# Performance work log

Measured on AMD Instinct MI355X. Metric: run time of the kernel, lower is better.

The kernel has to match this reference:

```python
import jax, jax.numpy as jnp
import numpy as np

BN_EPS = 1e-5

def _conv3x3(x, w):
    # x: [N,C,H,W], w: [O,I,3,3], stride 1, padding 1, no bias
    return jax.lax.conv_general_dilated(
        x, w, window_strides=(1, 1), padding=((1, 1), (1, 1)),
        dimension_numbers=("NCHW", "OIHW", "NCHW"))

def _batchnorm(x, gamma, beta):
    # training-mode BN: batch statistics over (N,H,W)
    mean = jnp.mean(x, axis=(0, 2, 3), keepdims=True)
    var = jnp.mean(jnp.square(x - mean), axis=(0, 2, 3), keepdims=True)
    inv = jax.lax.rsqrt(var + BN_EPS)
    g = gamma.reshape(1, -1, 1, 1)
    b = beta.reshape(1, -1, 1, 1)
    return (x - mean) * inv * g + b

def setup_inputs() -> dict:
    key = jax.random.key(0)
    ks = jax.random.split(key, 3)
    x = jax.random.normal(ks[0], (32, 64, 128, 128), dtype=jnp.float32)
    # He-style scaled 3x3 conv kernels
    w1 = jax.random.normal(ks[1], (64, 64, 3, 3), dtype=jnp.float32) * (2.0 / (64 * 9)) ** 0.5
    w2 = jax.random.normal(ks[2], (64, 64, 3, 3), dtype=jnp.float32) * (2.0 / (64 * 9)) ** 0.5
    return {
        "x": x, "w1": w1, "w2": w2,
        "bn1_gamma": jnp.ones((64,), jnp.float32),
        "bn1_beta": jnp.zeros((64,), jnp.float32),
        "bn2_gamma": jnp.ones((64,), jnp.float32),
        "bn2_beta": jnp.zeros((64,), jnp.float32),
    }

def reference(x, w1, w2, bn1_gamma, bn1_beta, bn2_gamma, bn2_beta):
    out = _batchnorm(_conv3x3(x, w1), bn1_gamma, bn1_beta)
    out = _conv3x3(out, w2)
    out = out + x  # option 'A', stride=1, planes[2]==planes[0] -> identity shortcut
    return _batchnorm(out, bn2_gamma, bn2_beta)
```

## Files before the change

kernel.cpp:

```cpp
#include <hip/hip_runtime.h>
#include <hip/hip_bf16.h>

#define NB 32
#define CH 64
#define HH 128
#define WW 128
#define HW (HH*WW)
#define CHW (CH*HW)
#define NCHW (NB*CHW)
#define CNT_PER_CH ((float)(NB*HW))

typedef __attribute__((ext_vector_type(8)))  short short8;
typedef __attribute__((ext_vector_type(16))) float f32x16;

__device__ __forceinline__ unsigned short f2bf(float f) {
  unsigned u = __builtin_bit_cast(unsigned, f);
  u += 0x7fffu + ((u >> 16) & 1u);
  return (unsigned short)(u >> 16);
}

__device__ __forceinline__ void gld_lds16(const void* g, void* s) {
  __builtin_amdgcn_global_load_lds(
      (const __attribute__((address_space(1))) unsigned int*)g,
      (__attribute__((address_space(3))) unsigned int*)s, 16, 0, 0);
}

__global__ __launch_bounds__(256) void t1_pack(const float* __restrict__ x,
                                               unsigned short* __restrict__ xb) {
  __shared__ __align__(16) unsigned short tmp[CH * WW];
  const int bid = blockIdx.x;
  const int tid = threadIdx.x;
  const float* src = x + (size_t)(bid >> 7) * CHW + (size_t)(bid & 127) * WW;
  for (int i = tid; i < 2048; i += 256) {
    const int ci = i >> 5, wq = i & 31;
    const float4 v = *(const float4*)(src + (size_t)ci * HW + wq * 4);
    unsigned short* d = &tmp[ci * WW + wq * 4];
    d[0] = f2bf(v.x); d[1] = f2bf(v.y); d[2] = f2bf(v.z); d[3] = f2bf(v.w);
  }
  __syncthreads();
  unsigned short* dst = xb + (size_t)bid * 8192;
  for (int i = tid; i < 1024; i += 256) {
    const int cb = i >> 7, w = i & 127;
    const unsigned short* s = &tmp[cb * 8 * WW + w];
    uint4 o;
    o.x = (unsigned)s[0]      | ((unsigned)s[WW]     << 16);
    o.y = (unsigned)s[2*WW]   | ((unsigned)s[3*WW]   << 16);
    o.z = (unsigned)s[4*WW]   | ((unsigned)s[5*WW]   << 16);
    o.w = (unsigned)s[6*WW]   | ((unsigned)s[7*WW]   << 16);
    *(uint4*)(dst + ((size_t)cb * WW + w) * 8) = o;
  }
}

__global__ __launch_bounds__(256) void pack_w(const float* __restrict__ w,
                                              const float* __restrict__ s1,
                                              const float* __restrict__ b1,
                                              unsigned short* __restrict__ wpk,
                                              float* __restrict__ tabs) {
  const int tid = threadIdx.x;
  for (int idx = tid; idx < 36864; idx += 256) {
    const int f = idx >> 9, l = (idx >> 3) & 63, r = idx & 7;
    const int m = f & 1, kq = (f >> 1) & 3, t = f >> 3;
    const int co = (l & 31) + 32 * m;
    const int ci = kq * 16 + (l >> 5) * 8 + r;
    float v = w[co * 576 + ci * 9 + t];
    if (s1) v *= s1[ci];
    wpk[idx] = f2bf(v);
  }
  if (tabs != nullptr && tid < 64) {
    const int co = tid;
    float tb[9];
    for (int t = 0; t < 9; ++t) {
      float a = 0.f;
      for (int ci = 0; ci < 64; ++ci) a += w[co * 576 + ci * 9 + t] * b1[ci];
      tb[t] = a;
    }
    tabs[0*64+co] = tb[0]+tb[1]+tb[2]+tb[3]+tb[4]+tb[5]+tb[6]+tb[7]+tb[8];
    tabs[1*64+co] = tb[0]+tb[1]+tb[2];
    tabs[2*64+co] = tb[6]+tb[7]+tb[8];
    tabs[3*64+co] = tb[0]+tb[3]+tb[6];
    tabs[4*64+co] = tb[2]+tb[5]+tb[8];
    tabs[5*64+co] = tb[0]; tabs[6*64+co] = tb[2];
    tabs[7*64+co] = tb[6]; tabs[8*64+co] = tb[8];
  }
}

template <bool IS2>
__global__ __launch_bounds__(256, 2)
void conv_mfma(const unsigned short* __restrict__ inb,
               const unsigned short* __restrict__ wpack,
               const float* __restrict__ tabs,
               const float* __restrict__ resid,
               unsigned short* __restrict__ outb,
               float* __restrict__ outf,
               float* __restrict__ psum, float* __restrict__ psq) {
  __shared__ __align__(16) unsigned short A[3][8][130][8];
  const int tid = threadIdx.x, bid = blockIdx.x;
  const int n = bid >> 7, h = bid & 127;
  const int wv = tid >> 6, lane = tid & 63;
  const int half = lane >> 5, lp = lane & 31;
  const int m  = wv & 1;
  const int nb = (wv >> 1) << 1;

  for (int q = wv; q < 48; q += 4) {
    const int rr = q >> 4, cb = (q >> 1) & 7, w0 = (q & 1) << 6;
    const int hr = h - 1 + rr;
    if ((unsigned)hr < 128u) {
      const unsigned short* g =
          inb + ((((size_t)n * 128 + hr) * 8 + cb) << 10) + (size_t)(w0 + lane) * 8;
      gld_lds16(g, &A[rr][cb][1 + w0][0]);
    } else {
      *(uint4*)&A[rr][cb][1 + w0 + lane][0] = make_uint4(0, 0, 0, 0);
    }
  }
  if (tid < 48) {
    const int rr = tid >> 4, cb = (tid >> 1) & 7, s = (tid & 1) ? 129 : 0;
    *(uint4*)&A[rr][cb][s][0] = make_uint4(0, 0, 0, 0);
  }

  short8 wr[36];
#pragma unroll
  for (int i = 0; i < 36; ++i) {
    const int f = ((i >> 2) << 3) + ((i & 3) << 1) + m;
    wr[i] = *(const short8*)(wpack + (size_t)f * 512 + (size_t)lane * 8);
  }
  __syncthreads();

  f32x16 acc0 = {}; f32x16 acc1 = {};
#pragma unroll
  for (int kh = 0; kh < 3; ++kh) {
#pragma unroll
    for (int kw = 0; kw < 3; ++kw) {
#pragma unroll
      for (int kq = 0; kq < 4; ++kq) {
        const short8 wf = wr[(kh * 3 + kw) * 4 + kq];
        const int cb = kq * 2 + half;
        const short8 b0 = *(const short8*)&A[kh][cb][nb * 32 + lp + kw][0];
        const short8 b1 = *(const short8*)&A[kh][cb][(nb + 1) * 32 + lp + kw][0];
        acc0 = __builtin_amdgcn_mfma_f32_32x32x16_bf16(wf, b0, acc0, 0, 0, 0);
        acc1 = __builtin_amdgcn_mfma_f32_32x32x16_bf16(wf, b1, acc1, 0, 0, 0);
      }
    }
  }

  if (!IS2) {
    unsigned short* dst = outb + ((size_t)bid << 13);
#pragma unroll
    for (int nt = 0; nt < 2; ++nt) {
      const f32x16& a = nt ? acc1 : acc0;
      const int px = (nb + nt) * 32 + lp;
#pragma unroll
      for (int rq = 0; rq < 4; ++rq) {
        uint2 pk;
        pk.x = (unsigned)f2bf(a[rq*4+0]) | ((unsigned)f2bf(a[rq*4+1]) << 16);
        pk.y = (unsigned)f2bf(a[rq*4+2]) | ((unsigned)f2bf(a[rq*4+3]) << 16);
        *(uint2*)(dst + (((size_t)(rq + 4*m)) << 10) + (size_t)px * 8 + half * 4) = pk;
      }
    }
  } else {
    const bool bh0 = (h == 0), bh1 = (h == 127);
#pragma unroll
    for (int nt = 0; nt < 2; ++nt) {
      f32x16& a = nt ? acc1 : acc0;
      const int px = (nb + nt) * 32 + lp;
      const bool bw0 = (px == 0), bw1 = (px == 127);
#pragma unroll
      for (int r = 0; r < 16; ++r) {
        const int co = (r & 3) + ((r >> 2) << 3) + 4 * half + 32 * m;
        float tb = tabs[co];
        if (bh0) tb -= tabs[64 + co];
        if (bh1) tb -= tabs[128 + co];
        if (bw0) tb -= tabs[192 + co];
        if (bw1) tb -= tabs[256 + co];
        if (bh0 && bw0) tb += tabs[320 + co];
        if (bh0 && bw1) tb += tabs[384 + co];
        if (bh1 && bw0) tb += tabs[448 + co];
        if (bh1 && bw1) tb += tabs[512 + co];
        const size_t oi = (((size_t)n * 64 + co) * 128 + h) * 128 + px;
        const float v = a[r] + tb + resid[oi];
        outf[oi] = v;
        a[r] = v;
      }
    }
  }

#pragma unroll
  for (int r = 0; r < 16; ++r) {
    float s = acc0[r] + acc1[r];
    float q = acc0[r] * acc0[r] + acc1[r] * acc1[r];
    s += __shfl_xor(s, 1);  q += __shfl_xor(q, 1);
    s += __shfl_xor(s, 2);  q += __shfl_xor(q, 2);
    s += __shfl_xor(s, 4);  q += __shfl_xor(q, 4);
    s += __shfl_xor(s, 8);  q += __shfl_xor(q, 8);
    s += __shfl_xor(s, 16); q += __shfl_xor(q, 16);
    if (lp == 0) {
      const int co = (r & 3) + ((r >> 2) << 3) + 4 * half + 32 * m;
      atomicAdd(&psum[(bid & 63) * 64 + co], s);
      atomicAdd(&psq [(bid & 63) * 64 + co], q);
    }
  }
}

__global__ void finalize_bn(const float* __restrict__ psum, const float* __restrict__ psq,
                            const float* __restrict__ gamma, const float* __restrict__ beta,
                            float* __restrict__ scale, float* __restrict__ bias) {
  const int c = threadIdx.x;
  if (c < 64) {
    float s = 0.f, q = 0.f;
    for (int i = 0; i < 64; ++i) { s += psum[i * 64 + c]; q += psq[i * 64 + c]; }
    const float mean = s * (1.0f / CNT_PER_CH);
    const float var  = q * (1.0f / CNT_PER_CH) - mean * mean;
    const float inv  = rsqrtf(var + 1e-5f);
    const float sc   = inv * gamma[c];
    scale[c] = sc;
    bias[c]  = beta[c] - mean * sc;
  }
}

__global__ __launch_bounds__(256)
void apply_bn_k(float* __restrict__ out,
                const float* __restrict__ scale, const float* __restrict__ bias) {
  __shared__ float sc[CH], bs[CH];
  if (threadIdx.x < CH) { sc[threadIdx.x] = scale[threadIdx.x]; bs[threadIdx.x] = bias[threadIdx.x]; }
  __syncthreads();
  const size_t total4 = NCHW / 4;
  for (size_t i = (size_t)blockIdx.x * blockDim.x + threadIdx.x; i < total4;
       i += (size_t)gridDim.x * blockDim.x) {
    float4 v = reinterpret_cast<float4*>(out)[i];
    const int c = (int)(((i * 4) >> 14) & 63);
    const float s = sc[c], b = bs[c];
    v.x = fmaf(v.x, s, b);
    v.y = fmaf(v.y, s, b);
    v.z = fmaf(v.z, s, b);
    v.w = fmaf(v.w, s, b);
    reinterpret_cast<float4*>(out)[i] = v;
  }
}

extern "C" void kernel_launch(void* const* d_in, const int* in_sizes, int n_in,
                              void* d_out, int out_size, void* d_ws, size_t ws_size,
                              hipStream_t stream) {
  const float* x  = (const float*)d_in[0];
  const float* w1 = (const float*)d_in[1];
  const float* w2 = (const float*)d_in[2];
  const float* g1 = (const float*)d_in[3];
  const float* b1 = (const float*)d_in[4];
  const float* g2 = (const float*)d_in[5];
  const float* b2 = (const float*)d_in[6];
  float* out = (float*)d_out;
  char* ws = (char*)d_ws;

  unsigned short* XB  = (unsigned short*)ws;
  unsigned short* Y1B = (unsigned short*)(ws + 67108864);
  unsigned short* W2P = (unsigned short*)ws;
  float* TABS = (float*)(ws + 73728);
  float* SC1  = (float*)(ws + 76032);
  float* BS1  = (float*)(ws + 76288);
  float* SC2  = (float*)(ws + 76544);
  float* BS2  = (float*)(ws + 76800);
  float* P2S  = (float*)(ws + 77056);
  float* P2Q  = (float*)(ws + 93440);
  char* ob = (char*)d_out;
  unsigned short* W1P = (unsigned short*)ob;
  float* P1S = (float*)(ob + 73728);
  float* P1Q = (float*)(ob + 90112);

  hipMemsetAsync(ob + 73728, 0, 32768, stream);
  pack_w<<<1, 256, 0, stream>>>(w1, nullptr, nullptr, W1P, nullptr);
  t1_pack<<<4096, 256, 0, stream>>>(x, XB);
  conv_mfma<false><<<4096, 256, 0, stream>>>(XB, W1P, nullptr, nullptr,
                                             Y1B, nullptr, P1S, P1Q);
  finalize_bn<<<1, 64, 0, stream>>>(P1S, P1Q, g1, b1, SC1, BS1);
  hipMemsetAsync(ws + 77056, 0, 32768, stream);
  pack_w<<<1, 256, 0, stream>>>(w2, SC1, BS1, W2P, TABS);
  conv_mfma<true><<<4096, 256, 0, stream>>>(Y1B, W2P, TABS, x,
                                            nullptr, out, P2S, P2Q);
  finalize_bn<<<1, 64, 0, stream>>>(P2S, P2Q, g2, b2, SC2, BS2);
  apply_bn_k<<<2048, 256, 0, stream>>>(out, SC2, BS2);
}
```

Before: 575.0 us.

## Process four output rows per conv block with a rolling LDS row ring

Each conv block now computes four consecutive output rows instead of one. A 4-slot LDS ring keeps input rows resident, so each new row loads only one additional input row rather than three. The next row is prefetched during the current row's MFMA work, and residual values are loaded early. Per-block weight register loads are amortised over four rows. The trade-off is 4x fewer blocks, more dynamic LDS per block and a per-row barrier, which can reduce occupancy and tail balance.

```diff
diff --git a/kernel.cpp b/kernel.cpp
--- a/kernel.cpp
+++ b/kernel.cpp
@@ -9,6 +9,7 @@
 #define CHW (CH*HW)
 #define NCHW (NB*CHW)
 #define CNT_PER_CH ((float)(NB*HW))
+#define ROWS 4
 
 typedef __attribute__((ext_vector_type(8)))  short short8;
 typedef __attribute__((ext_vector_type(16))) float f32x16;
@@ -93,28 +94,34 @@
                unsigned short* __restrict__ outb,
                float* __restrict__ outf,
                float* __restrict__ psum, float* __restrict__ psq) {
-  __shared__ __align__(16) unsigned short A[3][8][130][8];
+  extern __shared__ __align__(16) unsigned short A[];
   const int tid = threadIdx.x, bid = blockIdx.x;
-  const int n = bid >> 7, h = bid & 127;
+  const int n = bid >> 5, h0 = (bid & 31) << 2;
   const int wv = tid >> 6, lane = tid & 63;
   const int half = lane >> 5, lp = lane & 31;
   const int m  = wv & 1;
   const int nb = (wv >> 1) << 1;
 
-  for (int q = wv; q < 48; q += 4) {
-    const int rr = q >> 4, cb = (q >> 1) & 7, w0 = (q & 1) << 6;
-    const int hr = h - 1 + rr;
-    if ((unsigned)hr < 128u) {
-      const unsigned short* g =
-          inb + ((((size_t)n * 128 + hr) * 8 + cb) << 10) + (size_t)(w0 + lane) * 8;
-      gld_lds16(g, &A[rr][cb][1 + w0][0]);
-    } else {
-      *(uint4*)&A[rr][cb][1 + w0 + lane][0] = make_uint4(0, 0, 0, 0);
-    }
-  }
-  if (tid < 48) {
-    const int rr = tid >> 4, cb = (tid >> 1) & 7, s = (tid & 1) ? 129 : 0;
-    *(uint4*)&A[rr][cb][s][0] = make_uint4(0, 0, 0, 0);
+  auto stage = [&](int ir) {
+    const int sl = (ir + 4) & 3;
+#pragma unroll
+    for (int t = 0; t < 4; ++t) {
+      const int id = wv + 4 * t;
+      const int cb = id >> 1, wh = id & 1;
+      unsigned short* dst = &A[(((sl * 8 + cb) * 130) + 1 + wh * 64) * 8];
+      if ((unsigned)ir < 128u) {
+        const unsigned short* g = inb + ((((size_t)n * 128 + ir) * 8 + cb) << 10)
+                                      + (size_t)(wh * 64 + lane) * 8;
+        gld_lds16(g, dst);
+      } else {
+        *(uint4*)(dst + (size_t)lane * 8) = make_uint4(0, 0, 0, 0);
+      }
+    }
+  };
+
+  if (tid < 64) {
+    const int sl = tid >> 4, cb = (tid >> 1) & 7, s = (tid & 1) ? 129 : 0;
+    *(uint4*)&A[(((sl * 8 + cb) * 130) + s) * 8] = make_uint4(0, 0, 0, 0);
   }
 
   short8 wr[36];
@@ -123,79 +130,103 @@
     const int f = ((i >> 2) << 3) + ((i & 3) << 1) + m;
     wr[i] = *(const short8*)(wpack + (size_t)f * 512 + (size_t)lane * 8);
   }
-  __syncthreads();
-
-  f32x16 acc0 = {}; f32x16 acc1 = {};
-#pragma unroll
-  for (int kh = 0; kh < 3; ++kh) {
-#pragma unroll
-    for (int kw = 0; kw < 3; ++kw) {
-#pragma unroll
-      for (int kq = 0; kq < 4; ++kq) {
-        const short8 wf = wr[(kh * 3 + kw) * 4 + kq];
-        const int cb = kq * 2 + half;
-        const short8 b0 = *(const short8*)&A[kh][cb][nb * 32 + lp + kw][0];
-        const short8 b1 = *(const short8*)&A[kh][cb][(nb + 1) * 32 + lp + kw][0];
-        acc0 = __builtin_amdgcn_mfma_f32_32x32x16_bf16(wf, b0, acc0, 0, 0, 0);
-        acc1 = __builtin_amdgcn_mfma_f32_32x32x16_bf16(wf, b1, acc1, 0, 0, 0);
-      }
-    }
-  }
-
-  if (!IS2) {
-    unsigned short* dst = outb + ((size_t)bid << 13);
-#pragma unroll
-    for (int nt = 0; nt < 2; ++nt) {
-      const f32x16& a = nt ? acc1 : acc0;
-      const int px = (nb + nt) * 32 + lp;
-#pragma unroll
-      for (int rq = 0; rq < 4; ++rq) {
-        uint2 pk;
-        pk.x = (unsigned)f2bf(a[rq*4+0]) | ((unsigned)f2bf(a[rq*4+1]) << 16);
-        pk.y = (unsigned)f2bf(a[rq*4+2]) | ((unsigned)f2bf(a[rq*4+3]) << 16);
-        *(uint2*)(dst + (((size_t)(rq + 4*m)) << 10) + (size_t)px * 8 + half * 4) = pk;
-      }
-    }
-  } else {
-    const bool bh0 = (h == 0), bh1 = (h == 127);
-#pragma unroll
-    for (int nt = 0; nt < 2; ++nt) {
-      f32x16& a = nt ? acc1 : acc0;
-      const int px = (nb + nt) * 32 + lp;
-      const bool bw0 = (px == 0), bw1 = (px == 127);
-#pragma unroll
-      for (int r = 0; r < 16; ++r) {
-        const int co = (r & 3) + ((r >> 2) << 3) + 4 * half + 32 * m;
-        float tb = tabs[co];
-        if (bh0) tb -= tabs[64 + co];
-        if (bh1) tb -= tabs[128 + co];
-        if (bw0) tb -= tabs[192 + co];
-        if (bw1) tb -= tabs[256 + co];
-        if (bh0 && bw0) tb += tabs[320 + co];
-        if (bh0 && bw1) tb += tabs[384 + co];
-        if (bh1 && bw0) tb += tabs[448 + co];
-        if (bh1 && bw1) tb += tabs[512 + co];
-        const size_t oi = (((size_t)n * 64 + co) * 128 + h) * 128 + px;
-        const float v = a[r] + tb + resid[oi];
-        outf[oi] = v;
-        a[r] = v;
-      }
-    }
-  }
-
-#pragma unroll
-  for (int r = 0; r < 16; ++r) {
-    float s = acc0[r] + acc1[r];
-    float q = acc0[r] * acc0[r] + acc1[r] * acc1[r];
-    s += __shfl_xor(s, 1);  q += __shfl_xor(q, 1);
-    s += __shfl_xor(s, 2);  q += __shfl_xor(q, 2);
-    s += __shfl_xor(s, 4);  q += __shfl_xor(q, 4);
-    s += __shfl_xor(s, 8);  q += __shfl_xor(q, 8);
-    s += __shfl_xor(s, 16); q += __shfl_xor(q, 16);
-    if (lp == 0) {
-      const int co = (r & 3) + ((r >> 2) << 3) + 4 * half + 32 * m;
-      atomicAdd(&psum[(bid & 63) * 64 + co], s);
-      atomicAdd(&psq [(bid & 63) * 64 + co], q);
+
+  stage(h0 - 1); stage(h0); stage(h0 + 1);
+
+  for (int k = 0; k < ROWS; ++k) {
+    const int r = h0 + k;
+    __syncthreads();
+
+    float rv[2][16];
+    if (IS2) {
+#pragma unroll
+      for (int nt = 0; nt < 2; ++nt) {
+        const int px = (nb + nt) * 32 + lp;
+#pragma unroll
+        for (int rr = 0; rr < 16; ++rr) {
+          const int co = (rr & 3) + ((rr >> 2) << 3) + 4 * half + 32 * m;
+          rv[nt][rr] = resid[(((size_t)n * 64 + co) * 128 + r) * 128 + px];
+        }
+      }
+    }
+
+    if (k < ROWS - 1) stage(r + 2);
+
+    const int sl_m1 = (r + 3) & 3, sl_0 = (r + 4) & 3, sl_p1 = (r + 5) & 3;
+    const int slot[3] = {sl_m1, sl_0, sl_p1};
+    f32x16 acc0 = {}; f32x16 acc1 = {};
+#pragma unroll
+    for (int kh = 0; kh < 3; ++kh) {
+      const int sb = slot[kh] * 8;
+#pragma unroll
+      for (int kw = 0; kw < 3; ++kw) {
+#pragma unroll
+        for (int kq = 0; kq < 4; ++kq) {
+          const short8 wf = wr[(kh * 3 + kw) * 4 + kq];
+          const int cb = kq * 2 + half;
+          const unsigned short* base = &A[((sb + cb) * 130) * 8];
+          const short8 b0 = *(const short8*)&base[(nb * 32 + lp + kw) * 8];
+          const short8 b1 = *(const short8*)&base[((nb + 1) * 32 + lp + kw) * 8];
+          acc0 = __builtin_amdgcn_mfma_f32_32x32x16_bf16(wf, b0, acc0, 0, 0, 0);
+          acc1 = __builtin_amdgcn_mfma_f32_32x32x16_bf16(wf, b1, acc1, 0, 0, 0);
+        }
+      }
+    }
+
+    if (!IS2) {
+      unsigned short* dst = outb + (((size_t)n * 128 + r) << 13);
+#pragma unroll
+      for (int nt = 0; nt < 2; ++nt) {
+        const f32x16& a = nt ? acc1 : acc0;
+        const int px = (nb + nt) * 32 + lp;
+#pragma unroll
+        for (int rq = 0; rq < 4; ++rq) {
+          uint2 pk;
+          pk.x = (unsigned)f2bf(a[rq*4+0]) | ((unsigned)f2bf(a[rq*4+1]) << 16);
+          pk.y = (unsigned)f2bf(a[rq*4+2]) | ((unsigned)f2bf(a[rq*4+3]) << 16);
+          *(uint2*)(dst + (((size_t)(rq + 4*m)) << 10) + (size_t)px * 8 + half * 4) = pk;
+        }
+      }
+    } else {
+      const bool bh0 = (r == 0), bh1 = (r == 127);
+#pragma unroll
+      for (int nt = 0; nt < 2; ++nt) {
+        f32x16& a = nt ? acc1 : acc0;
+        const int px = (nb + nt) * 32 + lp;
+        const bool bw0 = (px == 0), bw1 = (px == 127);
+#pragma unroll
+        for (int rr = 0; rr < 16; ++rr) {
+          const int co = (rr & 3) + ((rr >> 2) << 3) + 4 * half + 32 * m;
+          float tb = tabs[co];
+          if (bh0) tb -= tabs[64 + co];
+          if (bh1) tb -= tabs[128 + co];
+          if (bw0) tb -= tabs[192 + co];
+          if (bw1) tb -= tabs[256 + co];
+          if (bh0 && bw0) tb += tabs[320 + co];
+          if (bh0 && bw1) tb += tabs[384 + co];
+          if (bh1 && bw0) tb += tabs[448 + co];
+          if (bh1 && bw1) tb += tabs[512 + co];
+          const float v = a[rr] + tb + rv[nt][rr];
+          outf[(((size_t)n * 64 + co) * 128 + r) * 128 + px] = v;
+          a[rr] = v;
+        }
+      }
+    }
+
+#pragma unroll
+    for (int rr = 0; rr < 16; ++rr) {
+      float s = acc0[rr] + acc1[rr];
+      float q = acc0[rr] * acc0[rr] + acc1[rr] * acc1[rr];
+      s += __shfl_xor(s, 1);  q += __shfl_xor(q, 1);
+      s += __shfl_xor(s, 2);  q += __shfl_xor(q, 2);
+      s += __shfl_xor(s, 4);  q += __shfl_xor(q, 4);
+      s += __shfl_xor(s, 8);  q += __shfl_xor(q, 8);
+      s += __shfl_xor(s, 16); q += __shfl_xor(q, 16);
+      if (lp == 0) {
+        const int co = (rr & 3) + ((rr >> 2) << 3) + 4 * half + 32 * m;
+        atomicAdd(&psum[(bid & 63) * 64 + co], s);
+        atomicAdd(&psq [(bid & 63) * 64 + co], q);
+      }
     }
   }
 }
@@ -264,16 +295,18 @@
   float* P1S = (float*)(ob + 73728);
   float* P1Q = (float*)(ob + 90112);
 
+  const size_t conv_lds = 4 * 8 * 130 * 8 * sizeof(unsigned short);
+
   hipMemsetAsync(ob + 73728, 0, 32768, stream);
   pack_w<<<1, 256, 0, stream>>>(w1, nullptr, nullptr, W1P, nullptr);
   t1_pack<<<4096, 256, 0, stream>>>(x, XB);
-  conv_mfma<false><<<4096, 256, 0, stream>>>(XB, W1P, nullptr, nullptr,
-                                             Y1B, nullptr, P1S, P1Q);
+  conv_mfma<false><<<1024, 256, conv_lds, stream>>>(XB, W1P, nullptr, nullptr,
+                                                    Y1B, nullptr, P1S, P1Q);
   finalize_bn<<<1, 64, 0, stream>>>(P1S, P1Q, g1, b1, SC1, BS1);
   hipMemsetAsync(ws + 77056, 0, 32768, stream);
   pack_w<<<1, 256, 0, stream>>>(w2, SC1, BS1, W2P, TABS);
-  conv_mfma<true><<<4096, 256, 0, stream>>>(Y1B, W2P, TABS, x,
-                                            nullptr, out, P2S, P2Q);
+  conv_mfma<true><<<1024, 256, conv_lds, stream>>>(Y1B, W2P, TABS, x,
+                                                   nullptr, out, P2S, P2Q);
   finalize_bn<<<1, 64, 0, stream>>>(P2S, P2Q, g2, b2, SC2, BS2);
   apply_bn_k<<<2048, 256, 0, stream>>>(out, SC2, BS2);
 }
```

Measured after the change: 559.1 us. -2.8%, faster.

## Replace LDS-staged conv with single-wave blocks streaming operands from global memory

Applied to the files above, without the earlier changes.

The conv kernel drops the shared-memory row staging and register-resident weights. Each 64-thread block now handles a 32-pixel segment of one output row and loads its input fragments and weight fragments straight from global memory (relying on cache), with a swizzled block index. BN partial-stat slots grow from 64 to 256 to reduce atomic contention, and finalize_bn uses 256 threads to sum the slots. This trades LDS reuse and barrier cost for more blocks and more global/L2 traffic; weights are reloaded per MFMA step.

```diff
diff --git a/kernel.cpp b/kernel.cpp
--- a/kernel.cpp
+++ b/kernel.cpp
@@ -9,6 +9,7 @@
 #define CHW (CH*HW)
 #define NCHW (NB*CHW)
 #define CNT_PER_CH ((float)(NB*HW))
+#define SLOTS 256
 
 typedef __attribute__((ext_vector_type(8)))  short short8;
 typedef __attribute__((ext_vector_type(16))) float f32x16;
@@ -17,12 +18,6 @@
   unsigned u = __builtin_bit_cast(unsigned, f);
   u += 0x7fffu + ((u >> 16) & 1u);
   return (unsigned short)(u >> 16);
-}
-
-__device__ __forceinline__ void gld_lds16(const void* g, void* s) {
-  __builtin_amdgcn_global_load_lds(
-      (const __attribute__((address_space(1))) unsigned int*)g,
-      (__attribute__((address_space(3))) unsigned int*)s, 16, 0, 0);
 }
 
 __global__ __launch_bounds__(256) void t1_pack(const float* __restrict__ x,
@@ -85,87 +80,73 @@
 }
 
 template <bool IS2>
-__global__ __launch_bounds__(256, 2)
-void conv_mfma(const unsigned short* __restrict__ inb,
-               const unsigned short* __restrict__ wpack,
-               const float* __restrict__ tabs,
-               const float* __restrict__ resid,
-               unsigned short* __restrict__ outb,
-               float* __restrict__ outf,
-               float* __restrict__ psum, float* __restrict__ psq) {
-  __shared__ __align__(16) unsigned short A[3][8][130][8];
-  const int tid = threadIdx.x, bid = blockIdx.x;
-  const int n = bid >> 7, h = bid & 127;
-  const int wv = tid >> 6, lane = tid & 63;
+__global__ __launch_bounds__(64, 3)
+void conv_stream(const unsigned short* __restrict__ inb,
+                 const unsigned short* __restrict__ wpack,
+                 const float* __restrict__ tabs,
+                 const float* __restrict__ resid,
+                 unsigned short* __restrict__ outb,
+                 float* __restrict__ outf,
+                 float* __restrict__ psum, float* __restrict__ psq) {
+  const int b = blockIdx.x;
+  const int vid = ((b & 7) << 11) | (b >> 3);
+  const int seg = vid & 3;
+  const int h   = (vid >> 2) & 127;
+  const int n   = vid >> 9;
+  const int lane = threadIdx.x;
   const int half = lane >> 5, lp = lane & 31;
-  const int m  = wv & 1;
-  const int nb = (wv >> 1) << 1;
-
-  for (int q = wv; q < 48; q += 4) {
-    const int rr = q >> 4, cb = (q >> 1) & 7, w0 = (q & 1) << 6;
-    const int hr = h - 1 + rr;
-    if ((unsigned)hr < 128u) {
-      const unsigned short* g =
-          inb + ((((size_t)n * 128 + hr) * 8 + cb) << 10) + (size_t)(w0 + lane) * 8;
-      gld_lds16(g, &A[rr][cb][1 + w0][0]);
-    } else {
-      *(uint4*)&A[rr][cb][1 + w0 + lane][0] = make_uint4(0, 0, 0, 0);
-    }
-  }
-  if (tid < 48) {
-    const int rr = tid >> 4, cb = (tid >> 1) & 7, s = (tid & 1) ? 129 : 0;
-    *(uint4*)&A[rr][cb][s][0] = make_uint4(0, 0, 0, 0);
-  }
-
-  short8 wr[36];
-#pragma unroll
-  for (int i = 0; i < 36; ++i) {
-    const int f = ((i >> 2) << 3) + ((i & 3) << 1) + m;
-    wr[i] = *(const short8*)(wpack + (size_t)f * 512 + (size_t)lane * 8);
-  }
-  __syncthreads();
+  const int px = (seg << 5) + lp;
 
   f32x16 acc0 = {}; f32x16 acc1 = {};
+  const unsigned short* nbase = inb + (size_t)n * (128 * 8192);
+
 #pragma unroll
   for (int kh = 0; kh < 3; ++kh) {
+    const int hr = h + kh - 1;
+    if ((unsigned)hr >= 128u) continue;
+    const unsigned short* rb = nbase + (size_t)hr * 8192;
 #pragma unroll
     for (int kw = 0; kw < 3; ++kw) {
+      const int pxs = px + kw - 1;
+      const bool wok = (unsigned)pxs < 128u;
+      const int pxc = pxs < 0 ? 0 : (pxs > 127 ? 127 : pxs);
 #pragma unroll
       for (int kq = 0; kq < 4; ++kq) {
-        const short8 wf = wr[(kh * 3 + kw) * 4 + kq];
-        const int cb = kq * 2 + half;
-        const short8 b0 = *(const short8*)&A[kh][cb][nb * 32 + lp + kw][0];
-        const short8 b1 = *(const short8*)&A[kh][cb][(nb + 1) * 32 + lp + kw][0];
-        acc0 = __builtin_amdgcn_mfma_f32_32x32x16_bf16(wf, b0, acc0, 0, 0, 0);
-        acc1 = __builtin_amdgcn_mfma_f32_32x32x16_bf16(wf, b1, acc1, 0, 0, 0);
+        const int cb = (kq << 1) + half;
+        short8 bf = *(const short8*)(rb + ((size_t)cb << 10) + ((size_t)pxc << 3));
+        short8 zz = {};
+        if (!wok) bf = zz;
+        const int f = (((kh * 3 + kw) << 2) + kq) << 1;
+        const short8 w0 = *(const short8*)(wpack + ((size_t)f << 9) + ((size_t)lane << 3));
+        const short8 w1 = *(const short8*)(wpack + ((size_t)(f + 1) << 9) + ((size_t)lane << 3));
+        acc0 = __builtin_amdgcn_mfma_f32_32x32x16_bf16(w0, bf, acc0, 0, 0, 0);
+        acc1 = __builtin_amdgcn_mfma_f32_32x32x16_bf16(w1, bf, acc1, 0, 0, 0);
       }
     }
   }
 
   if (!IS2) {
-    unsigned short* dst = outb + ((size_t)bid << 13);
-#pragma unroll
-    for (int nt = 0; nt < 2; ++nt) {
-      const f32x16& a = nt ? acc1 : acc0;
-      const int px = (nb + nt) * 32 + lp;
+    unsigned short* dst = outb + (size_t)(n * 128 + h) * 8192;
+#pragma unroll
+    for (int m = 0; m < 2; ++m) {
+      const f32x16& a = m ? acc1 : acc0;
 #pragma unroll
       for (int rq = 0; rq < 4; ++rq) {
         uint2 pk;
         pk.x = (unsigned)f2bf(a[rq*4+0]) | ((unsigned)f2bf(a[rq*4+1]) << 16);
         pk.y = (unsigned)f2bf(a[rq*4+2]) | ((unsigned)f2bf(a[rq*4+3]) << 16);
-        *(uint2*)(dst + (((size_t)(rq + 4*m)) << 10) + (size_t)px * 8 + half * 4) = pk;
+        *(uint2*)(dst + (((size_t)(rq + (m << 2))) << 10) + ((size_t)px << 3) + (half << 2)) = pk;
       }
     }
   } else {
     const bool bh0 = (h == 0), bh1 = (h == 127);
-#pragma unroll
-    for (int nt = 0; nt < 2; ++nt) {
-      f32x16& a = nt ? acc1 : acc0;
-      const int px = (nb + nt) * 32 + lp;
-      const bool bw0 = (px == 0), bw1 = (px == 127);
+    const bool bw0 = (px == 0), bw1 = (px == 127);
+#pragma unroll
+    for (int m = 0; m < 2; ++m) {
+      f32x16& a = m ? acc1 : acc0;
 #pragma unroll
       for (int r = 0; r < 16; ++r) {
-        const int co = (r & 3) + ((r >> 2) << 3) + 4 * half + 32 * m;
+        const int co = (r & 3) + ((r >> 2) << 3) + (half << 2) + (m << 5);
         float tb = tabs[co];
         if (bh0) tb -= tabs[64 + co];
         if (bh1) tb -= tabs[128 + co];
@@ -175,7 +156,7 @@
         if (bh0 && bw1) tb += tabs[384 + co];
         if (bh1 && bw0) tb += tabs[448 + co];
         if (bh1 && bw1) tb += tabs[512 + co];
-        const size_t oi = (((size_t)n * 64 + co) * 128 + h) * 128 + px;
+        const size_t oi = (((size_t)(n * 64 + co)) * 128 + h) * 128 + px;
         const float v = a[r] + tb + resid[oi];
         outf[oi] = v;
         a[r] = v;
@@ -183,30 +164,43 @@
     }
   }
 
-#pragma unroll
-  for (int r = 0; r < 16; ++r) {
-    float s = acc0[r] + acc1[r];
-    float q = acc0[r] * acc0[r] + acc1[r] * acc1[r];
-    s += __shfl_xor(s, 1);  q += __shfl_xor(q, 1);
-    s += __shfl_xor(s, 2);  q += __shfl_xor(q, 2);
-    s += __shfl_xor(s, 4);  q += __shfl_xor(q, 4);
-    s += __shfl_xor(s, 8);  q += __shfl_xor(q, 8);
-    s += __shfl_xor(s, 16); q += __shfl_xor(q, 16);
-    if (lp == 0) {
-      const int co = (r & 3) + ((r >> 2) << 3) + 4 * half + 32 * m;
-      atomicAdd(&psum[(bid & 63) * 64 + co], s);
-      atomicAdd(&psq [(bid & 63) * 64 + co], q);
-    }
-  }
-}
-
-__global__ void finalize_bn(const float* __restrict__ psum, const float* __restrict__ psq,
-                            const float* __restrict__ gamma, const float* __restrict__ beta,
-                            float* __restrict__ scale, float* __restrict__ bias) {
-  const int c = threadIdx.x;
-  if (c < 64) {
-    float s = 0.f, q = 0.f;
-    for (int i = 0; i < 64; ++i) { s += psum[i * 64 + c]; q += psq[i * 64 + c]; }
+  const int slot = vid & (SLOTS - 1);
+#pragma unroll
+  for (int m = 0; m < 2; ++m) {
+    const f32x16& a = m ? acc1 : acc0;
+#pragma unroll
+    for (int r = 0; r < 16; ++r) {
+      float s = a[r], q = a[r] * a[r];
+      s += __shfl_xor(s, 1);  q += __shfl_xor(q, 1);
+      s += __shfl_xor(s, 2);  q += __shfl_xor(q, 2);
+      s += __shfl_xor(s, 4);  q += __shfl_xor(q, 4);
+      s += __shfl_xor(s, 8);  q += __shfl_xor(q, 8);
+      s += __shfl_xor(s, 16); q += __shfl_xor(q, 16);
+      if (lp == 0) {
+        const int co = (r & 3) + ((r >> 2) << 3) + (half << 2) + (m << 5);
+        atomicAdd(&psum[slot * 64 + co], s);
+        atomicAdd(&psq [slot * 64 + co], q);
+      }
+    }
+  }
+}
+
+__global__ __launch_bounds__(256)
+void finalize_bn(const float* __restrict__ psum, const float* __restrict__ psq,
+                 const float* __restrict__ gamma, const float* __restrict__ beta,
+                 float* __restrict__ scale, float* __restrict__ bias) {
+  __shared__ float ls[4][64], lq[4][64];
+  const int c = threadIdx.x & 63, sg = threadIdx.x >> 6;
+  float s = 0.f, q = 0.f;
+  for (int i = sg * (SLOTS / 4); i < (sg + 1) * (SLOTS / 4); ++i) {
+    s += psum[(size_t)i * 64 + c];
+    q += psq[(size_t)i * 64 + c];
+  }
+  ls[sg][c] = s; lq[sg][c] = q;
+  __syncthreads();
+  if (threadIdx.x < 64) {
+    s = ls[0][c] + ls[1][c] + ls[2][c] + ls[3][c];
+    q = lq[0][c] + lq[1][c] + lq[2][c] + lq[3][c];
     const float mean = s * (1.0f / CNT_PER_CH);
     const float var  = q * (1.0f / CNT_PER_CH) - mean * mean;
     const float inv  = rsqrtf(var + 1e-5f);
@@ -257,23 +251,23 @@
   float* BS1  = (float*)(ws + 76288);
   float* SC2  = (float*)(ws + 76544);
   float* BS2  = (float*)(ws + 76800);
-  float* P2S  = (float*)(ws + 77056);
-  float* P2Q  = (float*)(ws + 93440);
+  float* P2S  = (float*)(ws + 131072);
+  float* P2Q  = (float*)(ws + 131072 + 65536);
   char* ob = (char*)d_out;
   unsigned short* W1P = (unsigned short*)ob;
   float* P1S = (float*)(ob + 73728);
-  float* P1Q = (float*)(ob + 90112);
-
-  hipMemsetAsync(ob + 73728, 0, 32768, stream);
+  float* P1Q = (float*)(ob + 73728 + 65536);
+
   pack_w<<<1, 256, 0, stream>>>(w1, nullptr, nullptr, W1P, nullptr);
+  hipMemsetAsync(ob + 73728, 0, 131072, stream);
   t1_pack<<<4096, 256, 0, stream>>>(x, XB);
-  conv_mfma<false><<<4096, 256, 0, stream>>>(XB, W1P, nullptr, nullptr,
-                                             Y1B, nullptr, P1S, P1Q);
-  finalize_bn<<<1, 64, 0, stream>>>(P1S, P1Q, g1, b1, SC1, BS1);
-  hipMemsetAsync(ws + 77056, 0, 32768, stream);
+  conv_stream<false><<<16384, 64, 0, stream>>>(XB, W1P, nullptr, nullptr,
+                                               Y1B, nullptr, P1S, P1Q);
+  finalize_bn<<<1, 256, 0, stream>>>(P1S, P1Q, g1, b1, SC1, BS1);
+  hipMemsetAsync(ws + 131072, 0, 131072, stream);
   pack_w<<<1, 256, 0, stream>>>(w2, SC1, BS1, W2P, TABS);
-  conv_mfma<true><<<4096, 256, 0, stream>>>(Y1B, W2P, TABS, x,
-                                            nullptr, out, P2S, P2Q);
-  finalize_bn<<<1, 64, 0, stream>>>(P2S, P2Q, g2, b2, SC2, BS2);
+  conv_stream<true><<<16384, 64, 0, stream>>>(Y1B, W2P, TABS, x,
+                                              nullptr, out, P2S, P2Q);
+  finalize_bn<<<1, 256, 0, stream>>>(P2S, P2Q, g2, b2, SC2, BS2);
   apply_bn_k<<<2048, 256, 0, stream>>>(out, SC2, BS2);
 }
```

Result: faster. 550.9 us (-4.2%).
